# Performance work log

Measured on AMD Instinct MI355X. Metric: run time of the kernel, lower is better.

Reference implementation:

```python
import jax, jax.numpy as jnp
import numpy as np

B, S, IN, OUT = 8, 2048, 1024, 4096
QMAX = 255.0  # 2**8 - 1 levels for 8-bit


def _quantize(x):
    """Per-tensor affine int8 quantization, matching Int8Linear.quantize."""
    x_max = x.max()
    x_min = x.min()
    scale = (x_max - x_min) / QMAX
    zero_point = jnp.round((x_max * -128.0 - x_min * 127.0) / (x_max - x_min))
    # torch does .to(torch.int8): wrapping cast; round has zero grad, int cast detaches
    x_q = jax.lax.stop_gradient((jnp.round(x / scale) + zero_point).astype(jnp.int8))
    return x_q, scale, zero_point


def setup_inputs() -> dict:
    key = jax.random.key(0)
    kx, kw, kb = jax.random.split(key, 3)
    x = jax.random.normal(kx, (B, S, IN), dtype=jnp.float32)
    w = jax.random.normal(kw, (OUT, IN), dtype=jnp.float32) * 0.02  # nn.Linear-ish init scale
    w_q, w_scale, w_zp = _quantize(w)  # done once at module init in torch
    bias = jax.random.normal(kb, (OUT,), dtype=jnp.float32) * 0.01
    return {
        "x": x,
        "w_q": w_q.astype(jnp.int32),  # stored int8 values, carried as int32
        "w_scale": w_scale,
        "w_zp": w_zp,
        "bias": bias,
    }


def reference(x, w_q, w_scale, w_zp, bias):
    # quantize activation per call (per-tensor affine)
    x_q, x_scale, x_zp = _quantize(x)
    # torch: matmul(x_q.to(int32) - x_zero_point, weight.T.to(int32) - zero_point)
    # zero points are FLOAT tensors, so the subtraction promotes to float32 and the
    # GEMM runs in float32 on centered integer-valued operands.
    xc = x_q.astype(jnp.float32) - x_zp            # [B, S, IN]
    wc = w_q.astype(jnp.float32) - w_zp            # [OUT, IN]
    acc = jnp.einsum('bsi,oi->bso', xc, wc)        # [B, S, OUT]
    return acc * (x_scale * w_scale) + bias
```

## Files before the change

kernel.cpp:

```cpp
#include <hip/hip_runtime.h>
#include <stdint.h>

#define M_ROWS 16384
#define N_COLS 4096
#define K_DIM  1024

typedef __bf16 bf16x8 __attribute__((ext_vector_type(8)));
typedef float  f32x4  __attribute__((ext_vector_type(4)));

__device__ __forceinline__ void gload_lds16(const void* g, void* l) {
    __builtin_amdgcn_global_load_lds(
        (const __attribute__((address_space(1))) unsigned int*)g,
        (__attribute__((address_space(3))) unsigned int*)l, 16, 0, 0);
}

__device__ __forceinline__ unsigned short f32_to_bf16_exact(float f) {
    return (unsigned short)(__builtin_bit_cast(unsigned int, f) >> 16);
}

__global__ void k_minmax(const float4* __restrict__ x,
                         float* __restrict__ pmax, float* __restrict__ pmin) {
    const int n4 = (M_ROWS * K_DIM) / 4;
    float mx = -3.402823466e38f, mn = 3.402823466e38f;
    for (int i = blockIdx.x * blockDim.x + threadIdx.x; i < n4;
         i += gridDim.x * blockDim.x) {
        float4 v = x[i];
        mx = fmaxf(mx, fmaxf(fmaxf(v.x, v.y), fmaxf(v.z, v.w)));
        mn = fminf(mn, fminf(fminf(v.x, v.y), fminf(v.z, v.w)));
    }
#pragma unroll
    for (int off = 32; off > 0; off >>= 1) {
        mx = fmaxf(mx, __shfl_xor(mx, off));
        mn = fminf(mn, __shfl_xor(mn, off));
    }
    __shared__ float smx[4], smn[4];
    const int wave = threadIdx.x >> 6, lane = threadIdx.x & 63;
    if (lane == 0) { smx[wave] = mx; smn[wave] = mn; }
    __syncthreads();
    if (threadIdx.x == 0) {
        mx = fmaxf(fmaxf(smx[0], smx[1]), fmaxf(smx[2], smx[3]));
        mn = fminf(fminf(smn[0], smn[1]), fminf(smn[2], smn[3]));
        pmax[blockIdx.x] = mx;
        pmin[blockIdx.x] = mn;
    }
}

__global__ void k_scalars(const float* __restrict__ pmax, const float* __restrict__ pmin,
                          const float* __restrict__ w_scale, float* __restrict__ scal) {
    float mx = -3.402823466e38f, mn = 3.402823466e38f;
    for (int i = threadIdx.x; i < 2048; i += 256) {
        mx = fmaxf(mx, pmax[i]);
        mn = fminf(mn, pmin[i]);
    }
#pragma unroll
    for (int off = 32; off > 0; off >>= 1) {
        mx = fmaxf(mx, __shfl_xor(mx, off));
        mn = fminf(mn, __shfl_xor(mn, off));
    }
    __shared__ float smx[4], smn[4];
    const int wave = threadIdx.x >> 6, lane = threadIdx.x & 63;
    if (lane == 0) { smx[wave] = mx; smn[wave] = mn; }
    __syncthreads();
    if (threadIdx.x == 0) {
        mx = fmaxf(fmaxf(smx[0], smx[1]), fmaxf(smx[2], smx[3]));
        mn = fminf(fminf(smn[0], smn[1]), fminf(smn[2], smn[3]));
        const float scale = (mx - mn) / 255.0f;
        const float zp = rintf((mx * -128.0f - mn * 127.0f) / (mx - mn));
        scal[0] = scale;
        scal[1] = zp;
        scal[2] = scale * w_scale[0];
    }
}

__global__ void k_quant(const float4* __restrict__ x, const float* __restrict__ scal,
                        ushort4* __restrict__ xc) {
    const float scale = scal[0], zp = scal[1];
    const int n4 = (M_ROWS * K_DIM) / 4;
    for (int i = blockIdx.x * blockDim.x + threadIdx.x; i < n4;
         i += gridDim.x * blockDim.x) {
        float4 v = x[i];
        ushort4 o;
        {
            int q0 = (int)(rintf(v.x / scale) + zp);
            int q1 = (int)(rintf(v.y / scale) + zp);
            int q2 = (int)(rintf(v.z / scale) + zp);
            int q3 = (int)(rintf(v.w / scale) + zp);
            o.x = f32_to_bf16_exact((float)(signed char)q0 - zp);
            o.y = f32_to_bf16_exact((float)(signed char)q1 - zp);
            o.z = f32_to_bf16_exact((float)(signed char)q2 - zp);
            o.w = f32_to_bf16_exact((float)(signed char)q3 - zp);
        }
        xc[i] = o;
    }
}

__global__ void k_prepw(const int4* __restrict__ wq, const float* __restrict__ wzp,
                        ushort4* __restrict__ wc) {
    const float zp = wzp[0];
    const int n4 = (N_COLS * K_DIM) / 4;
    for (int i = blockIdx.x * blockDim.x + threadIdx.x; i < n4;
         i += gridDim.x * blockDim.x) {
        int4 v = wq[i];
        ushort4 o;
        o.x = f32_to_bf16_exact((float)v.x - zp);
        o.y = f32_to_bf16_exact((float)v.y - zp);
        o.z = f32_to_bf16_exact((float)v.z - zp);
        o.w = f32_to_bf16_exact((float)v.w - zp);
        wc[i] = o;
    }
}

__global__ void k_gemm(const unsigned short* __restrict__ A,
                       const unsigned short* __restrict__ B,
                       const float* __restrict__ scal,
                       const float* __restrict__ bias,
                       float* __restrict__ C) {
    __shared__ unsigned short As[128 * 64];
    __shared__ unsigned short Bs[128 * 64];

    const int tid = threadIdx.x;
    const int wave = tid >> 6, lane = tid & 63;

    const int wg = blockIdx.x;
    const int swz = ((wg & 7) << 9) | (wg >> 3);
    const int bm = swz >> 5;
    const int bn = swz & 31;

    f32x4 acc[4][4];
#pragma unroll
    for (int i = 0; i < 4; ++i)
#pragma unroll
        for (int j = 0; j < 4; ++j)
#pragma unroll
            for (int r = 0; r < 4; ++r) acc[i][j][r] = 0.0f;

    const char* Ab = (const char*)(A + (size_t)bm * 128 * K_DIM);
    const char* Bb = (const char*)(B + (size_t)bn * 128 * K_DIM);
    const int colb = (lane & 7) << 4;
    const int rsub = lane >> 3;

    const int wr  = (wave >> 1) << 6;
    const int wc2 = (wave & 1) << 6;
    const int fr  = lane & 15;
    const int kg  = lane >> 4;

    for (int kt = 0; kt < K_DIM / 64; ++kt) {
        const int kb = kt * 128;
#pragma unroll
        for (int c = 0; c < 4; ++c) {
            const int chunk = c * 4 + wave;
            const int row = (chunk << 3) + rsub;
            const int lin = chunk << 10;
            gload_lds16(Ab + (size_t)row * 2048 + kb + colb, (char*)As + lin);
            gload_lds16(Bb + (size_t)row * 2048 + kb + colb, (char*)Bs + lin);
        }
        asm volatile("s_waitcnt vmcnt(0)" ::: "memory");
        __syncthreads();

#pragma unroll
        for (int kk = 0; kk < 2; ++kk) {
            bf16x8 af[4], bf[4];
#pragma unroll
            for (int i = 0; i < 4; ++i) {
                af[i] = *(const bf16x8*)(As + (wr  + i * 16 + fr) * 64 + kk * 32 + kg * 8);
                bf[i] = *(const bf16x8*)(Bs + (wc2 + i * 16 + fr) * 64 + kk * 32 + kg * 8);
            }
#pragma unroll
            for (int i = 0; i < 4; ++i)
#pragma unroll
                for (int j = 0; j < 4; ++j)
                    acc[i][j] = __builtin_amdgcn_mfma_f32_16x16x32_bf16(
                        af[i], bf[j], acc[i][j], 0, 0, 0);
        }
        __syncthreads();
    }

    const float alpha = scal[2];
#pragma unroll
    for (int j = 0; j < 4; ++j) {
        const int gn = bn * 128 + wc2 + j * 16 + fr;
        const float bv = bias[gn];
#pragma unroll
        for (int i = 0; i < 4; ++i) {
            const int gm0 = bm * 128 + wr + i * 16 + kg * 4;
#pragma unroll
            for (int r = 0; r < 4; ++r)
                C[(size_t)(gm0 + r) * N_COLS + gn] = acc[i][j][r] * alpha + bv;
        }
    }
}

extern "C" void kernel_launch(void* const* d_in, const int* in_sizes, int n_in,
                              void* d_out, int out_size, void* d_ws, size_t ws_size,
                              hipStream_t stream) {
    const float* x    = (const float*)d_in[0];
    const int*   wq   = (const int*)d_in[1];
    const float* wsc  = (const float*)d_in[2];
    const float* wzp  = (const float*)d_in[3];
    const float* bias = (const float*)d_in[4];
    float* out = (float*)d_out;

    char* ws = (char*)d_ws;
    unsigned short* xc = (unsigned short*)(ws);
    unsigned short* wc = (unsigned short*)(ws + 33554432);
    float* pmax = (float*)(ws + 41943040);
    float* pmin = (float*)(ws + 41951232);
    float* scal = (float*)(ws + 41959424);

    k_prepw  <<<2048, 256, 0, stream>>>((const int4*)wq, wzp, (ushort4*)wc);
    k_minmax <<<2048, 256, 0, stream>>>((const float4*)x, pmax, pmin);
    k_scalars<<<1,    256, 0, stream>>>(pmax, pmin, wsc, scal);
    k_quant  <<<2048, 256, 0, stream>>>((const float4*)x, scal, (ushort4*)xc);
    k_gemm   <<<4096, 256, 0, stream>>>(xc, wc, scal, bias, out);
}
```

Measured before the change: 493.2 us.

## Rewrite GEMM with 256x256 tiles, double-buffered LDS prefetch and XOR swizzle

The GEMM kernel moves from 128x128 tiles with 4 waves to 256x256 tiles with 8 waves. It double-buffers A and B in 128KB of LDS, issuing global-to-LDS loads for later k-tiles while MFMAs run on the current one. LDS columns are XOR-swizzled to avoid bank conflicts, and the compute is split into quarter phases with barriers and raised wave priority. The aim is to hide global-load latency and raise arithmetic intensity, at the cost of heavy LDS use, more accumulator registers, and a tight, fragile wait/barrier schedule.

```diff
diff --git a/kernel.cpp b/kernel.cpp
--- a/kernel.cpp
+++ b/kernel.cpp
@@ -4,6 +4,7 @@
 #define M_ROWS 16384
 #define N_COLS 4096
 #define K_DIM  1024
+#define NT     (K_DIM / 64)
 
 typedef __bf16 bf16x8 __attribute__((ext_vector_type(8)));
 typedef float  f32x4  __attribute__((ext_vector_type(4)));
@@ -13,6 +14,10 @@
         (const __attribute__((address_space(1))) unsigned int*)g,
         (__attribute__((address_space(3))) unsigned int*)l, 16, 0, 0);
 }
+
+#define SBAR() do { __builtin_amdgcn_sched_barrier(0); \
+                    __builtin_amdgcn_s_barrier();      \
+                    __builtin_amdgcn_sched_barrier(0); } while (0)
 
 __device__ __forceinline__ unsigned short f32_to_bf16_exact(float f) {
     return (unsigned short)(__builtin_bit_cast(unsigned int, f) >> 16);
@@ -80,16 +85,14 @@
          i += gridDim.x * blockDim.x) {
         float4 v = x[i];
         ushort4 o;
-        {
-            int q0 = (int)(rintf(v.x / scale) + zp);
-            int q1 = (int)(rintf(v.y / scale) + zp);
-            int q2 = (int)(rintf(v.z / scale) + zp);
-            int q3 = (int)(rintf(v.w / scale) + zp);
-            o.x = f32_to_bf16_exact((float)(signed char)q0 - zp);
-            o.y = f32_to_bf16_exact((float)(signed char)q1 - zp);
-            o.z = f32_to_bf16_exact((float)(signed char)q2 - zp);
-            o.w = f32_to_bf16_exact((float)(signed char)q3 - zp);
-        }
+        int q0 = (int)(rintf(v.x / scale) + zp);
+        int q1 = (int)(rintf(v.y / scale) + zp);
+        int q2 = (int)(rintf(v.z / scale) + zp);
+        int q3 = (int)(rintf(v.w / scale) + zp);
+        o.x = f32_to_bf16_exact((float)(signed char)q0 - zp);
+        o.y = f32_to_bf16_exact((float)(signed char)q1 - zp);
+        o.z = f32_to_bf16_exact((float)(signed char)q2 - zp);
+        o.w = f32_to_bf16_exact((float)(signed char)q3 - zp);
         xc[i] = o;
     }
 }
@@ -110,84 +113,118 @@
     }
 }
 
-__global__ void k_gemm(const unsigned short* __restrict__ A,
-                       const unsigned short* __restrict__ B,
-                       const float* __restrict__ scal,
-                       const float* __restrict__ bias,
-                       float* __restrict__ C) {
-    __shared__ unsigned short As[128 * 64];
-    __shared__ unsigned short Bs[128 * 64];
-
-    const int tid = threadIdx.x;
+__global__ __launch_bounds__(512, 2)
+void k_gemm(const unsigned short* __restrict__ A,
+            const unsigned short* __restrict__ B,
+            const float* __restrict__ scal,
+            const float* __restrict__ bias,
+            float* __restrict__ C) {
+    __shared__ char lds[131072];
+
+    const int tid  = threadIdx.x;
     const int wave = tid >> 6, lane = tid & 63;
-
-    const int wg = blockIdx.x;
-    const int swz = ((wg & 7) << 9) | (wg >> 3);
-    const int bm = swz >> 5;
-    const int bn = swz & 31;
-
-    f32x4 acc[4][4];
-#pragma unroll
-    for (int i = 0; i < 4; ++i)
-#pragma unroll
-        for (int j = 0; j < 4; ++j)
-#pragma unroll
-            for (int r = 0; r < 4; ++r) acc[i][j][r] = 0.0f;
-
-    const char* Ab = (const char*)(A + (size_t)bm * 128 * K_DIM);
-    const char* Bb = (const char*)(B + (size_t)bn * 128 * K_DIM);
-    const int colb = (lane & 7) << 4;
-    const int rsub = lane >> 3;
-
-    const int wr  = (wave >> 1) << 6;
-    const int wc2 = (wave & 1) << 6;
-    const int fr  = lane & 15;
-    const int kg  = lane >> 4;
-
-    for (int kt = 0; kt < K_DIM / 64; ++kt) {
-        const int kb = kt * 128;
-#pragma unroll
-        for (int c = 0; c < 4; ++c) {
-            const int chunk = c * 4 + wave;
-            const int row = (chunk << 3) + rsub;
-            const int lin = chunk << 10;
-            gload_lds16(Ab + (size_t)row * 2048 + kb + colb, (char*)As + lin);
-            gload_lds16(Bb + (size_t)row * 2048 + kb + colb, (char*)Bs + lin);
+    const int wm = wave >> 2, wn = wave & 3;
+    const int fr = lane & 15, kg = lane >> 4;
+
+    const int wg  = blockIdx.x;
+    const int swz = ((wg & 7) << 7) | (wg >> 3);
+    const int bm  = swz >> 4;
+    const int bn  = swz & 15;
+
+    const int scol = ((tid & 7) ^ ((tid >> 3) & 7)) << 4;
+    const char* gA = (const char*)A + (size_t)(bm * 256 + (tid >> 3)) * (K_DIM * 2) + scol;
+    const char* gB = (const char*)B + (size_t)(bn * 256 + (tid >> 3)) * (K_DIM * 2) + scol;
+
+#define STAGE_A(tt, h, b) do {                                          \
+        const char* g_ = gA + (size_t)(tt) * 128 + (size_t)(h) * 262144; \
+        char* l_ = lds + (b) * 32768 + (h) * 16384 + wave * 1024;        \
+        gload_lds16(g_, l_);                                             \
+        gload_lds16(g_ + 131072, l_ + 8192);                             \
+    } while (0)
+#define STAGE_B(tt, h, b) do {                                          \
+        const char* g_ = gB + (size_t)(tt) * 128 + (size_t)(h) * 262144; \
+        char* l_ = lds + 65536 + (b) * 32768 + (h) * 16384 + wave * 1024; \
+        gload_lds16(g_, l_);                                             \
+        gload_lds16(g_ + 131072, l_ + 8192);                             \
+    } while (0)
+
+    const int kx0 = ((kg * 16) ^ ((fr & 7) << 4));
+    const int kx1 = ((64 + kg * 16) ^ ((fr & 7) << 4));
+    const int arow = (wm * 128 + fr) * 128;
+    const int brow = (wn * 64 + fr) * 128;
+
+    f32x4 acc[8][4] = {};
+    bf16x8 bf[4][2];
+
+    STAGE_A(0, 0, 0); STAGE_A(0, 1, 0);
+    STAGE_B(0, 0, 0); STAGE_B(0, 1, 0);
+    STAGE_B(1, 0, 1); STAGE_B(1, 1, 1);
+    asm volatile("s_waitcnt vmcnt(4)" ::: "memory");
+    SBAR();
+
+    for (int t = 0; t < NT; ++t) {
+        const int b = t & 1;
+        const char* Ab = lds + b * 32768;
+        const char* Bb = lds + 65536 + b * 32768;
+#pragma unroll
+        for (int q = 0; q < 4; ++q) {
+            bf16x8 af[2][2];
+            if (q == 0) {
+#pragma unroll
+                for (int j = 0; j < 4; ++j) {
+                    bf[j][0] = *(const bf16x8*)(Bb + brow + j * 2048 + kx0);
+                    bf[j][1] = *(const bf16x8*)(Bb + brow + j * 2048 + kx1);
+                }
+            }
+#pragma unroll
+            for (int i2 = 0; i2 < 2; ++i2) {
+                const int i = 2 * q + i2;
+                af[i2][0] = *(const bf16x8*)(Ab + arow + i * 2048 + kx0);
+                af[i2][1] = *(const bf16x8*)(Ab + arow + i * 2048 + kx1);
+            }
+            if (q == 0)      { if (t + 1 < NT) STAGE_A(t + 1, 0, b ^ 1); }
+            else if (q == 1) { if (t + 1 < NT) STAGE_A(t + 1, 1, b ^ 1); }
+            else if (q == 2) { if (t + 2 < NT) STAGE_B(t + 2, 0, b); }
+            else {
+                if (t + 2 < NT) {
+                    STAGE_B(t + 2, 1, b);
+                    asm volatile("s_waitcnt vmcnt(4)" ::: "memory");
+                } else {
+                    asm volatile("s_waitcnt vmcnt(0)" ::: "memory");
+                }
+            }
+            SBAR();
+            __builtin_amdgcn_s_setprio(1);
+#pragma unroll
+            for (int kk = 0; kk < 2; ++kk)
+#pragma unroll
+                for (int i2 = 0; i2 < 2; ++i2)
+#pragma unroll
+                    for (int j = 0; j < 4; ++j)
+                        acc[2 * q + i2][j] = __builtin_amdgcn_mfma_f32_16x16x32_bf16(
+                            af[i2][kk], bf[j][kk], acc[2 * q + i2][j], 0, 0, 0);
+            __builtin_amdgcn_s_setprio(0);
+            SBAR();
         }
-        asm volatile("s_waitcnt vmcnt(0)" ::: "memory");
-        __syncthreads();
-
-#pragma unroll
-        for (int kk = 0; kk < 2; ++kk) {
-            bf16x8 af[4], bf[4];
-#pragma unroll
-            for (int i = 0; i < 4; ++i) {
-                af[i] = *(const bf16x8*)(As + (wr  + i * 16 + fr) * 64 + kk * 32 + kg * 8);
-                bf[i] = *(const bf16x8*)(Bs + (wc2 + i * 16 + fr) * 64 + kk * 32 + kg * 8);
-            }
-#pragma unroll
-            for (int i = 0; i < 4; ++i)
-#pragma unroll
-                for (int j = 0; j < 4; ++j)
-                    acc[i][j] = __builtin_amdgcn_mfma_f32_16x16x32_bf16(
-                        af[i], bf[j], acc[i][j], 0, 0, 0);
+    }
+
+    const float alpha = scal[2];
+    const int gc_base = bn * 256 + wn * 64;
+    const int gr_base = bm * 256 + wm * 128;
+#pragma unroll
+    for (int j = 0; j < 4; ++j) {
+        const int gc = gc_base + j * 16 + fr;
+        const float bv = bias[gc];
+#pragma unroll
+        for (int i = 0; i < 8; ++i) {
+            const int gr0 = gr_base + i * 16 + kg * 4;
+#pragma unroll
+            for (int r = 0; r < 4; ++r)
+                C[(size_t)(gr0 + r) * N_COLS + gc] = acc[i][j][r] * alpha + bv;
         }
-        __syncthreads();
-    }
-
-    const float alpha = scal[2];
-#pragma unroll
-    for (int j = 0; j < 4; ++j) {
-        const int gn = bn * 128 + wc2 + j * 16 + fr;
-        const float bv = bias[gn];
-#pragma unroll
-        for (int i = 0; i < 4; ++i) {
-            const int gm0 = bm * 128 + wr + i * 16 + kg * 4;
-#pragma unroll
-            for (int r = 0; r < 4; ++r)
-                C[(size_t)(gm0 + r) * N_COLS + gn] = acc[i][j][r] * alpha + bv;
-        }
-    }
+    }
+#undef STAGE_A
+#undef STAGE_B
 }
 
 extern "C" void kernel_launch(void* const* d_in, const int* in_sizes, int n_in,
@@ -211,5 +248,5 @@
     k_minmax <<<2048, 256, 0, stream>>>((const float4*)x, pmax, pmin);
     k_scalars<<<1,    256, 0, stream>>>(pmax, pmin, wsc, scal);
     k_quant  <<<2048, 256, 0, stream>>>((const float4*)x, scal, (ushort4*)xc);
-    k_gemm   <<<4096, 256, 0, stream>>>(xc, wc, scal, bias, out);
-}
+    k_gemm   <<<1024, 512, 0, stream>>>(xc, wc, scal, bias, out);
+}
```

New measurement: 469.9 us. 4.7% less time.
